# Kernel tuning notes

Hardware: AMD Instinct MI355X
Metric: run time of the kernel (lower is better)

Reference implementation:

```python
import jax, jax.numpy as jnp
import numpy as np

D_MODEL = 2048
N_HEADS = 16
D_HEAD = D_MODEL // N_HEADS
BASE = 10000.0


def _rope_cos_sin(T, d_head, base, dtype=jnp.float32):
    half = d_head // 2
    inv_freq = 1.0 / (base ** (jnp.arange(half, dtype=jnp.float32) * 2.0 / d_head))
    angles = jnp.arange(T, dtype=jnp.float32)[:, None] * inv_freq[None, :]  # [T, half]
    return jnp.cos(angles).astype(dtype), jnp.sin(angles).astype(dtype)


def _apply_rope(x, cos, sin):
    # x: [B, H, T, d_head]; cos/sin: [T, d_head//2]; interleaved pairs (0::2, 1::2)
    x1 = x[..., 0::2]
    x2 = x[..., 1::2]
    r1 = x1 * cos - x2 * sin
    r2 = x1 * sin + x2 * cos
    return jnp.stack([r1, r2], axis=-1).reshape(x.shape)


def setup_inputs() -> dict:
    key = jax.random.key(0)
    k1, k2, k3 = jax.random.split(key, 3)
    B, T = 2, 2048
    x = jax.random.normal(k1, (B, T, D_MODEL), dtype=jnp.float32)
    w_qkv = jax.random.normal(k2, (3 * D_MODEL, D_MODEL), dtype=jnp.float32) * 0.02
    w_out = jax.random.normal(k3, (D_MODEL, D_MODEL), dtype=jnp.float32) * 0.02
    return {"x": x, "w_qkv": w_qkv, "w_out": w_out}


def reference(x, w_qkv, w_out) -> jnp.ndarray:
    B, T, D = x.shape
    scale = D_HEAD ** -0.5
    qkv = jnp.einsum('btd,ed->bte', x, w_qkv)  # [B, T, 3D]
    q, k, v = jnp.split(qkv, 3, axis=-1)
    # [B, T, D] -> [B, H, T, d_head]
    q = q.reshape(B, T, N_HEADS, D_HEAD).transpose(0, 2, 1, 3)
    k = k.reshape(B, T, N_HEADS, D_HEAD).transpose(0, 2, 1, 3)
    v = v.reshape(B, T, N_HEADS, D_HEAD).transpose(0, 2, 1, 3)
    cos, sin = _rope_cos_sin(T, D_HEAD, BASE, dtype=x.dtype)
    q = _apply_rope(q, cos, sin)
    k = _apply_rope(k, cos, sin)
    scores = jnp.einsum('bhqd,bhkd->bhqk', q, k) * scale
    causal = jnp.tril(jnp.ones((T, T), dtype=bool))
    scores = jnp.where(causal, scores, jnp.finfo(scores.dtype).min)
    attn = jax.nn.softmax(scores, axis=-1)
    out = jnp.einsum('bhqk,bhkd->bhqd', attn, v)
    out = out.transpose(0, 2, 1, 3).reshape(B, T, D)
    return jnp.einsum('btd,ed->bte', out, w_out)
```

## Files before the change

### kernel.cpp

```cpp
#include <hip/hip_runtime.h>
#include <hip/hip_bf16.h>

typedef __attribute__((ext_vector_type(4))) float f32x4;
typedef __attribute__((ext_vector_type(8))) short short8;
typedef __attribute__((ext_vector_type(4))) unsigned short ushx4;

#define B_SZ 2
#define T_SZ 2048
#define H_SZ 16
#define DH 128
#define DM 2048
#define M_SZ 4096
#define N1 6144
#define KD 2048

static __device__ __forceinline__ unsigned short f2bf(float f) {
  union { float f; unsigned int u; } v; v.f = f;
  unsigned int r = v.u + 0x7fffu + ((v.u >> 16) & 1u);
  return (unsigned short)(r >> 16);
}
static __device__ __forceinline__ float bf2f(unsigned int u) {
  union { unsigned int u; float f; } v; v.u = u << 16; return v.f;
}

#define ASYNC_COPY16(gsrc, ldst) \
  __builtin_amdgcn_global_load_lds((const __attribute__((address_space(1))) void*)(gsrc), \
                                   (__attribute__((address_space(3))) void*)(ldst), 16, 0, 0)

__global__ __launch_bounds__(256) void cast_f32_bf16(const float* __restrict__ in,
                                                     unsigned short* __restrict__ out, int n4) {
  int i = blockIdx.x * 256 + threadIdx.x;
  if (i >= n4) return;
  float4 v = ((const float4*)in)[i];
  ushx4 o;
  o[0] = f2bf(v.x); o[1] = f2bf(v.y); o[2] = f2bf(v.z); o[3] = f2bf(v.w);
  ((ushx4*)out)[i] = o;
}

__global__ __launch_bounds__(64) void rope_table(float* __restrict__ cosb, float* __restrict__ sinb) {
  int t = blockIdx.x;
  int i = threadIdx.x;
  float inv = powf(10000.0f, -(float)i / 64.0f);
  float ang = (float)t * inv;
  cosb[t * 64 + i] = cosf(ang);
  sinb[t * 64 + i] = sinf(ang);
}

template <bool BF16OUT>
__global__ __launch_bounds__(256) void gemm_bt(const unsigned short* __restrict__ A,
                                               const unsigned short* __restrict__ Bt,
                                               void* __restrict__ Cout,
                                               int M, int N, int K) {
  __shared__ unsigned short As[128 * 32];
  __shared__ unsigned short Bs[128 * 32];
  const int tid = threadIdx.x;
  const int lane = tid & 63;
  const int wave = tid >> 6;
  const int wm = wave >> 1, wn = wave & 1;
  const int m0 = blockIdx.y * 128, n0 = blockIdx.x * 128;
  const int r = lane & 15, q = lane >> 4;

  f32x4 acc[4][4];
#pragma unroll
  for (int i = 0; i < 4; i++)
#pragma unroll
    for (int j = 0; j < 4; j++) acc[i][j] = (f32x4)0.0f;

  const int c0 = tid, c1 = tid + 256;
  const int row0 = c0 >> 2, kc0 = c0 & 3;
  const int row1 = c1 >> 2, kc1 = c1 & 3;

  for (int k0 = 0; k0 < K; k0 += 32) {
    __syncthreads();
    ASYNC_COPY16(A + (size_t)(m0 + row0) * K + k0 + kc0 * 8, &As[c0 * 8]);
    ASYNC_COPY16(A + (size_t)(m0 + row1) * K + k0 + kc1 * 8, &As[c1 * 8]);
    ASYNC_COPY16(Bt + (size_t)(n0 + row0) * K + k0 + kc0 * 8, &Bs[c0 * 8]);
    ASYNC_COPY16(Bt + (size_t)(n0 + row1) * K + k0 + kc1 * 8, &Bs[c1 * 8]);
    __syncthreads();

    short8 a[4], b[4];
#pragma unroll
    for (int mf = 0; mf < 4; mf++)
      a[mf] = *(const short8*)&As[(wm * 64 + mf * 16 + r) * 32 + q * 8];
#pragma unroll
    for (int nf = 0; nf < 4; nf++)
      b[nf] = *(const short8*)&Bs[(wn * 64 + nf * 16 + r) * 32 + q * 8];
#pragma unroll
    for (int mf = 0; mf < 4; mf++)
#pragma unroll
      for (int nf = 0; nf < 4; nf++)
        acc[mf][nf] = __builtin_amdgcn_mfma_f32_16x16x32_bf16(a[mf], b[nf], acc[mf][nf], 0, 0, 0);
  }

#pragma unroll
  for (int mf = 0; mf < 4; mf++) {
#pragma unroll
    for (int nf = 0; nf < 4; nf++) {
#pragma unroll
      for (int reg = 0; reg < 4; reg++) {
        int row = m0 + wm * 64 + mf * 16 + q * 4 + reg;
        int col = n0 + wn * 64 + nf * 16 + r;
        if (BF16OUT)
          ((unsigned short*)Cout)[(size_t)row * N + col] = f2bf(acc[mf][nf][reg]);
        else
          ((float*)Cout)[(size_t)row * N + col] = acc[mf][nf][reg];
      }
    }
  }
}

__global__ __launch_bounds__(256) void rope_scatter_qk(const unsigned short* __restrict__ qkv,
                                                       const float* __restrict__ cosb,
                                                       const float* __restrict__ sinb,
                                                       unsigned short* __restrict__ qb,
                                                       unsigned short* __restrict__ kb) {
  int idx = blockIdx.x * 256 + threadIdx.x;
  int m = idx >> 10;
  int p = idx & 1023;
  int h = p >> 6, i = p & 63;
  int t = m & (T_SZ - 1);
  int b = m >> 11;
  float c = cosb[t * 64 + i], s = sinb[t * 64 + i];
  size_t dst = (((size_t)(b * H_SZ + h) * T_SZ + t) * DH) + 2 * i;

  unsigned int v = *(const unsigned int*)&qkv[(size_t)m * N1 + h * DH + 2 * i];
  float x1 = bf2f(v & 0xffffu), x2 = bf2f(v >> 16);
  float r1 = x1 * c - x2 * s, r2 = x1 * s + x2 * c;
  *(unsigned int*)&qb[dst] = (unsigned int)f2bf(r1) | ((unsigned int)f2bf(r2) << 16);
  v = *(const unsigned int*)&qkv[(size_t)m * N1 + DM + h * DH + 2 * i];
  x1 = bf2f(v & 0xffffu); x2 = bf2f(v >> 16);
  r1 = x1 * c - x2 * s; r2 = x1 * s + x2 * c;
  *(unsigned int*)&kb[dst] = (unsigned int)f2bf(r1) | ((unsigned int)f2bf(r2) << 16);
}

__global__ __launch_bounds__(256) void v_transpose(const unsigned short* __restrict__ qkv,
                                                   unsigned short* __restrict__ vt) {
  __shared__ unsigned short tile[32][34];
  int bh = blockIdx.z, dblk = blockIdx.y, tblk = blockIdx.x;
  int b = bh >> 4, h = bh & 15;
  int tx = threadIdx.x & 31;
  int ty4 = threadIdx.x >> 5;
#pragma unroll
  for (int rr = 0; rr < 4; rr++) {
    int trow = ty4 * 4 + rr;
    int m = b * T_SZ + tblk * 32 + trow;
    tile[trow][tx] = qkv[(size_t)m * N1 + 2 * DM + h * DH + dblk * 32 + tx];
  }
  __syncthreads();
#pragma unroll
  for (int rr = 0; rr < 4; rr++) {
    int drow = ty4 * 4 + rr;
    vt[((size_t)bh * DH + dblk * 32 + drow) * T_SZ + tblk * 32 + tx] = tile[tx][drow];
  }
}

__global__ __launch_bounds__(256) void attn_fwd2(const unsigned short* __restrict__ qb,
                                                 const unsigned short* __restrict__ kb,
                                                 const unsigned short* __restrict__ vt,
                                                 unsigned short* __restrict__ of) {
  __shared__ unsigned short Ks[2][64 * 128];
  __shared__ unsigned short Vs[128 * 64];
  __shared__ unsigned short P_lds[4][16 * 72];

  const int tid = threadIdx.x;
  const int lane = tid & 63;
  const int w = tid >> 6;
  const int r = lane & 15, q = lane >> 4;
  const float scale = 0.08838834764831845f;

  int flat = blockIdx.x + 16 * blockIdx.y;
  int xcd = flat & 7;
  int j = flat >> 3;
  int bh = xcd * 4 + (j & 3);
  int qi = j >> 2;

  const int b = bh >> 4, h = bh & 15;
  const unsigned short* __restrict__ Qhead = qb + (size_t)bh * T_SZ * DH;
  const unsigned short* __restrict__ Kbase = kb + (size_t)bh * T_SZ * DH;
  const unsigned short* __restrict__ Vbase = vt + (size_t)bh * DH * T_SZ;

  auto stageK = [&](int kv0, int buf) {
#pragma unroll
    for (int p = 0; p < 4; p++) {
      int cc = p * 256 + tid;
      int row = cc >> 4, cr = cc & 15;
      ASYNC_COPY16(Kbase + (size_t)(kv0 + row) * DH + ((cr ^ (row & 7)) * 8),
                   &Ks[buf][cc * 8]);
    }
  };
  auto stageV = [&](int kv0) {
#pragma unroll
    for (int p = 0; p < 4; p++) {
      int cc = p * 256 + tid;
      int row = cc >> 3, cr = cc & 7;
      ASYNC_COPY16(Vbase + (size_t)row * T_SZ + kv0 + ((cr ^ (row & 7)) * 8),
                   &Vs[cc * 8]);
    }
  };

#pragma unroll 1
  for (int half = 0; half < 2; half++) {
    const int qtile = (half == 0) ? qi : (31 - qi);
    const int q0 = qtile * 64;
    const int qw = q0 + w * 16;
    const int nt = qtile + 1;

    int cur = 0;
    stageK(0, 0);

    short8 qf[4];
#pragma unroll
    for (int c = 0; c < 4; c++)
      qf[c] = *(const short8*)(Qhead + (size_t)(qw + r) * DH + c * 32 + q * 8);

    float m_run[4], l_run[4];
    f32x4 oacc[8];
#pragma unroll
    for (int i = 0; i < 4; i++) { m_run[i] = -1e30f; l_run[i] = 0.f; }
#pragma unroll
    for (int i = 0; i < 8; i++) oacc[i] = (f32x4)0.f;

#pragma unroll 1
    for (int t = 0; t < nt; t++) {
      const int kv0 = t * 64;
      stageV(kv0);
      if (t + 1 < nt) {
        stageK(kv0 + 64, cur ^ 1);
        asm volatile("s_waitcnt vmcnt(4)" ::: "memory");
      } else {
        asm volatile("s_waitcnt vmcnt(0)" ::: "memory");
      }
      __builtin_amdgcn_s_barrier();

      f32x4 S[4];
#pragma unroll
      for (int nf = 0; nf < 4; nf++) S[nf] = (f32x4)0.f;
#pragma unroll
      for (int nf = 0; nf < 4; nf++) {
#pragma unroll
        for (int c = 0; c < 4; c++) {
          short8 kf = *(const short8*)&Ks[cur][(nf * 16 + r) * 128 + (((c * 4 + q) ^ (r & 7)) * 8)];
          S[nf] = __builtin_amdgcn_mfma_f32_16x16x32_bf16(qf[c], kf, S[nf], 0, 0, 0);
        }
      }

      float Sv[4][4];
      const bool need_mask = (kv0 + 63 > qw);
#pragma unroll
      for (int nf = 0; nf < 4; nf++) {
#pragma unroll
        for (int reg = 0; reg < 4; reg++) {
          float v = S[nf][reg] * scale;
          if (need_mask) {
            int col = kv0 + nf * 16 + r;
            int row = qw + q * 4 + reg;
            if (col > row) v = -1e30f;
          }
          Sv[nf][reg] = v;
        }
      }

      float pmax[4], sc_old[4], rsum[4];
#pragma unroll
      for (int reg = 0; reg < 4; reg++) {
        float v = fmaxf(fmaxf(Sv[0][reg], Sv[1][reg]), fmaxf(Sv[2][reg], Sv[3][reg]));
#pragma unroll
        for (int s = 1; s < 16; s <<= 1) v = fmaxf(v, __shfl_xor(v, s));
        pmax[reg] = v;
      }
#pragma unroll
      for (int reg = 0; reg < 4; reg++) {
        float mn = fmaxf(m_run[reg], pmax[reg]);
        sc_old[reg] = __expf(m_run[reg] - mn);
        m_run[reg] = mn;
        rsum[reg] = 0.f;
      }
#pragma unroll
      for (int nf = 0; nf < 4; nf++) {
#pragma unroll
        for (int reg = 0; reg < 4; reg++) {
          float p = __expf(Sv[nf][reg] - m_run[reg]);
          rsum[reg] += p;
          P_lds[w][(q * 4 + reg) * 72 + nf * 16 + r] = f2bf(p);
        }
      }
#pragma unroll
      for (int reg = 0; reg < 4; reg++) {
        float v = rsum[reg];
#pragma unroll
        for (int s = 1; s < 16; s <<= 1) v += __shfl_xor(v, s);
        l_run[reg] = l_run[reg] * sc_old[reg] + v;
      }
#pragma unroll
      for (int df = 0; df < 8; df++)
#pragma unroll
        for (int reg = 0; reg < 4; reg++) oacc[df][reg] *= sc_old[reg];

      short8 pa[2];
#pragma unroll
      for (int kc = 0; kc < 2; kc++)
        pa[kc] = *(const short8*)&P_lds[w][r * 72 + kc * 32 + q * 8];
#pragma unroll
      for (int df = 0; df < 8; df++) {
#pragma unroll
        for (int kc = 0; kc < 2; kc++) {
          short8 vf = *(const short8*)&Vs[(df * 16 + r) * 64 + (((kc * 4 + q) ^ (r & 7)) * 8)];
          oacc[df] = __builtin_amdgcn_mfma_f32_16x16x32_bf16(pa[kc], vf, oacc[df], 0, 0, 0);
        }
      }

      __builtin_amdgcn_s_barrier();
      cur ^= 1;
    }

#pragma unroll
    for (int reg = 0; reg < 4; reg++) l_run[reg] = 1.0f / l_run[reg];
#pragma unroll
    for (int df = 0; df < 8; df++) {
#pragma unroll
      for (int reg = 0; reg < 4; reg++) {
        int row = qw + q * 4 + reg;
        int col = h * DH + df * 16 + r;
        of[((size_t)b * T_SZ + row) * DM + col] = f2bf(oacc[df][reg] * l_run[reg]);
      }
    }
  }
}

extern "C" void kernel_launch(void* const* d_in, const int* in_sizes, int n_in,
                              void* d_out, int out_size, void* d_ws, size_t ws_size,
                              hipStream_t stream) {
  (void)in_sizes; (void)n_in; (void)out_size; (void)ws_size;
  const float* x = (const float*)d_in[0];
  const float* w_qkv = (const float*)d_in[1];
  const float* w_out = (const float*)d_in[2];
  float* out = (float*)d_out;

  char* ws = (char*)d_ws;
  size_t off = 0;
  auto alloc = [&](size_t bytes) {
    char* p = ws + off;
    off += (bytes + 255) & ~(size_t)255;
    return p;
  };
  unsigned short* x_bf  = (unsigned short*)alloc((size_t)M_SZ * KD * 2);
  unsigned short* wq_bf = (unsigned short*)alloc((size_t)N1 * KD * 2);
  unsigned short* wo_bf = (unsigned short*)alloc((size_t)DM * KD * 2);
  unsigned short* qkv   = (unsigned short*)alloc((size_t)M_SZ * N1 * 2);
  unsigned short* qb    = (unsigned short*)alloc((size_t)B_SZ * H_SZ * T_SZ * DH * 2);
  unsigned short* kbuf  = (unsigned short*)alloc((size_t)B_SZ * H_SZ * T_SZ * DH * 2);
  unsigned short* vt    = (unsigned short*)alloc((size_t)B_SZ * H_SZ * DH * T_SZ * 2);
  unsigned short* oflat = (unsigned short*)alloc((size_t)M_SZ * DM * 2);
  float* cosb = (float*)alloc((size_t)T_SZ * 64 * 4);
  float* sinb = (float*)alloc((size_t)T_SZ * 64 * 4);

  cast_f32_bf16<<<8192, 256, 0, stream>>>(x, x_bf, M_SZ * KD / 4);
  cast_f32_bf16<<<12288, 256, 0, stream>>>(w_qkv, wq_bf, N1 * KD / 4);
  cast_f32_bf16<<<4096, 256, 0, stream>>>(w_out, wo_bf, DM * KD / 4);
  rope_table<<<T_SZ, 64, 0, stream>>>(cosb, sinb);

  gemm_bt<true><<<dim3(N1 / 128, M_SZ / 128), 256, 0, stream>>>(x_bf, wq_bf, qkv, M_SZ, N1, KD);

  rope_scatter_qk<<<16384, 256, 0, stream>>>(qkv, cosb, sinb, qb, kbuf);
  v_transpose<<<dim3(T_SZ / 32, 4, B_SZ * H_SZ), 256, 0, stream>>>(qkv, vt);

  attn_fwd2<<<dim3(16, 32), 256, 0, stream>>>(qb, kbuf, vt, oflat);

  gemm_bt<false><<<dim3(DM / 128, M_SZ / 128), 256, 0, stream>>>(oflat, wo_bf, out, M_SZ, DM, KD);
}
```

Measured before the change: 432.7 us.

## Replace GEMMs with 8-wave double-buffered ping-pong kernel using swizzled LDS and XCD remap

```diff
diff --git a/kernel.cpp b/kernel.cpp
--- a/kernel.cpp
+++ b/kernel.cpp
@@ -46,60 +46,162 @@
   sinb[t * 64 + i] = sinf(ang);
 }
 
-template <bool BF16OUT>
-__global__ __launch_bounds__(256) void gemm_bt(const unsigned short* __restrict__ A,
-                                               const unsigned short* __restrict__ Bt,
-                                               void* __restrict__ Cout,
-                                               int M, int N, int K) {
-  __shared__ unsigned short As[128 * 32];
-  __shared__ unsigned short Bs[128 * 32];
+template <int BN, bool BF16OUT>
+__global__ __launch_bounds__(512) void gemm8p(const unsigned short* __restrict__ A,
+                                              const unsigned short* __restrict__ Bt,
+                                              void* __restrict__ Cout,
+                                              int N, int nbx) {
+  constexpr int NF = BN / 64;
+  constexpr int LB = BN / 128;
+  constexpr int NT = KD / 64;
+  constexpr int WCOL = BN / 4;
+
+  __shared__ unsigned short As[2][2][256 * 32];
+  __shared__ unsigned short Bs[2][2][BN * 32];
+
   const int tid = threadIdx.x;
   const int lane = tid & 63;
-  const int wave = tid >> 6;
-  const int wm = wave >> 1, wn = wave & 1;
-  const int m0 = blockIdx.y * 128, n0 = blockIdx.x * 128;
+  const int w = tid >> 6;
+  const int wm = w >> 2, wn = w & 3;
   const int r = lane & 15, q = lane >> 4;
 
-  f32x4 acc[4][4];
-#pragma unroll
-  for (int i = 0; i < 4; i++)
-#pragma unroll
-    for (int j = 0; j < 4; j++) acc[i][j] = (f32x4)0.0f;
-
-  const int c0 = tid, c1 = tid + 256;
-  const int row0 = c0 >> 2, kc0 = c0 & 3;
-  const int row1 = c1 >> 2, kc1 = c1 & 3;
-
-  for (int k0 = 0; k0 < K; k0 += 32) {
-    __syncthreads();
-    ASYNC_COPY16(A + (size_t)(m0 + row0) * K + k0 + kc0 * 8, &As[c0 * 8]);
-    ASYNC_COPY16(A + (size_t)(m0 + row1) * K + k0 + kc1 * 8, &As[c1 * 8]);
-    ASYNC_COPY16(Bt + (size_t)(n0 + row0) * K + k0 + kc0 * 8, &Bs[c0 * 8]);
-    ASYNC_COPY16(Bt + (size_t)(n0 + row1) * K + k0 + kc1 * 8, &Bs[c1 * 8]);
-    __syncthreads();
-
-    short8 a[4], b[4];
+  const int cpx = gridDim.x >> 3;
+  const int f = (blockIdx.x & 7) * cpx + (blockIdx.x >> 3);
+  const int by = f / nbx, bx = f % nbx;
+  const int m0 = by * 256, n0 = bx * BN;
+
+  auto stageA = [&](int kt, int kh, int buf) {
+#pragma unroll
+    for (int l = 0; l < 2; l++) {
+      int cc = l * 512 + tid;
+      int row = cc >> 2, c = cc & 3;
+      ASYNC_COPY16(A + (size_t)(m0 + row) * KD + kt * 64 + kh * 32 + ((c ^ ((row >> 1) & 3)) * 8),
+                   &As[buf][kh][cc * 8]);
+    }
+  };
+  auto stageB = [&](int kt, int kh, int buf) {
+#pragma unroll
+    for (int l = 0; l < LB; l++) {
+      int cc = l * 512 + tid;
+      int row = cc >> 2, c = cc & 3;
+      ASYNC_COPY16(Bt + (size_t)(n0 + row) * KD + kt * 64 + kh * 32 + ((c ^ ((row >> 1) & 3)) * 8),
+                   &Bs[buf][kh][cc * 8]);
+    }
+  };
+
+  f32x4 acc[8][NF];
+#pragma unroll
+  for (int i = 0; i < 8; i++)
+#pragma unroll
+    for (int j = 0; j < NF; j++) acc[i][j] = (f32x4)0.0f;
+
+  short8 a[4], b[NF];
+
+  stageA(0, 0, 0); stageB(0, 0, 0); stageA(0, 1, 0); stageB(0, 1, 0);
+  if constexpr (BN == 256) asm volatile("s_waitcnt vmcnt(4)" ::: "memory");
+  else                     asm volatile("s_waitcnt vmcnt(3)" ::: "memory");
+  __builtin_amdgcn_s_barrier();
+
+#pragma unroll 1
+  for (int t = 0; t < NT; t++) {
+    const int buf = t & 1, nb = buf ^ 1;
+    const bool pf = (t + 1 < NT);
+
+#pragma unroll
+    for (int mf = 0; mf < 4; mf++) {
+      int row = wm * 128 + mf * 16 + r;
+      a[mf] = *(const short8*)&As[buf][0][row * 32 + ((q ^ ((row >> 1) & 3)) * 8)];
+    }
+#pragma unroll
+    for (int nf = 0; nf < NF; nf++) {
+      int row = wn * WCOL + nf * 16 + r;
+      b[nf] = *(const short8*)&Bs[buf][0][row * 32 + ((q ^ ((row >> 1) & 3)) * 8)];
+    }
+    if (pf) stageA(t + 1, 0, nb);
+    __builtin_amdgcn_s_barrier();
+    __builtin_amdgcn_s_setprio(1);
 #pragma unroll
     for (int mf = 0; mf < 4; mf++)
-      a[mf] = *(const short8*)&As[(wm * 64 + mf * 16 + r) * 32 + q * 8];
-#pragma unroll
-    for (int nf = 0; nf < 4; nf++)
-      b[nf] = *(const short8*)&Bs[(wn * 64 + nf * 16 + r) * 32 + q * 8];
+#pragma unroll
+      for (int nf = 0; nf < NF; nf++)
+        acc[mf][nf] = __builtin_amdgcn_mfma_f32_16x16x32_bf16(a[mf], b[nf], acc[mf][nf], 0, 0, 0);
+    __builtin_amdgcn_s_setprio(0);
+    __builtin_amdgcn_s_barrier();
+
+#pragma unroll
+    for (int mf = 0; mf < 4; mf++) {
+      int row = wm * 128 + 64 + mf * 16 + r;
+      a[mf] = *(const short8*)&As[buf][0][row * 32 + ((q ^ ((row >> 1) & 3)) * 8)];
+    }
+    if (pf) {
+      stageB(t + 1, 0, nb);
+      if constexpr (BN == 256) asm volatile("s_waitcnt vmcnt(4)" ::: "memory");
+      else                     asm volatile("s_waitcnt vmcnt(3)" ::: "memory");
+    } else {
+      asm volatile("s_waitcnt vmcnt(0)" ::: "memory");
+    }
+    __builtin_amdgcn_s_barrier();
+    __builtin_amdgcn_s_setprio(1);
 #pragma unroll
     for (int mf = 0; mf < 4; mf++)
 #pragma unroll
-      for (int nf = 0; nf < 4; nf++)
+      for (int nf = 0; nf < NF; nf++)
+        acc[4 + mf][nf] = __builtin_amdgcn_mfma_f32_16x16x32_bf16(a[mf], b[nf], acc[4 + mf][nf], 0, 0, 0);
+    __builtin_amdgcn_s_setprio(0);
+    __builtin_amdgcn_s_barrier();
+
+#pragma unroll
+    for (int mf = 0; mf < 4; mf++) {
+      int row = wm * 128 + mf * 16 + r;
+      a[mf] = *(const short8*)&As[buf][1][row * 32 + ((q ^ ((row >> 1) & 3)) * 8)];
+    }
+#pragma unroll
+    for (int nf = 0; nf < NF; nf++) {
+      int row = wn * WCOL + nf * 16 + r;
+      b[nf] = *(const short8*)&Bs[buf][1][row * 32 + ((q ^ ((row >> 1) & 3)) * 8)];
+    }
+    if (pf) stageA(t + 1, 1, nb);
+    __builtin_amdgcn_s_barrier();
+    __builtin_amdgcn_s_setprio(1);
+#pragma unroll
+    for (int mf = 0; mf < 4; mf++)
+#pragma unroll
+      for (int nf = 0; nf < NF; nf++)
         acc[mf][nf] = __builtin_amdgcn_mfma_f32_16x16x32_bf16(a[mf], b[nf], acc[mf][nf], 0, 0, 0);
+    __builtin_amdgcn_s_setprio(0);
+    __builtin_amdgcn_s_barrier();
+
+#pragma unroll
+    for (int mf = 0; mf < 4; mf++) {
+      int row = wm * 128 + 64 + mf * 16 + r;
+      a[mf] = *(const short8*)&As[buf][1][row * 32 + ((q ^ ((row >> 1) & 3)) * 8)];
+    }
+    if (pf) {
+      stageB(t + 1, 1, nb);
+      if constexpr (BN == 256) asm volatile("s_waitcnt vmcnt(4)" ::: "memory");
+      else                     asm volatile("s_waitcnt vmcnt(3)" ::: "memory");
+    } else {
+      asm volatile("s_waitcnt vmcnt(0)" ::: "memory");
+    }
+    __builtin_amdgcn_s_barrier();
+    __builtin_amdgcn_s_setprio(1);
+#pragma unroll
+    for (int mf = 0; mf < 4; mf++)
+#pragma unroll
+      for (int nf = 0; nf < NF; nf++)
+        acc[4 + mf][nf] = __builtin_amdgcn_mfma_f32_16x16x32_bf16(a[mf], b[nf], acc[4 + mf][nf], 0, 0, 0);
+    __builtin_amdgcn_s_setprio(0);
+    __builtin_amdgcn_s_barrier();
   }
 
 #pragma unroll
-  for (int mf = 0; mf < 4; mf++) {
-#pragma unroll
-    for (int nf = 0; nf < 4; nf++) {
+  for (int mf = 0; mf < 8; mf++) {
+#pragma unroll
+    for (int nf = 0; nf < NF; nf++) {
 #pragma unroll
       for (int reg = 0; reg < 4; reg++) {
-        int row = m0 + wm * 64 + mf * 16 + q * 4 + reg;
-        int col = n0 + wn * 64 + nf * 16 + r;
+        int row = m0 + wm * 128 + mf * 16 + q * 4 + reg;
+        int col = n0 + wn * WCOL + nf * 16 + r;
         if (BF16OUT)
           ((unsigned short*)Cout)[(size_t)row * N + col] = f2bf(acc[mf][nf][reg]);
         else
@@ -359,12 +461,12 @@
   cast_f32_bf16<<<4096, 256, 0, stream>>>(w_out, wo_bf, DM * KD / 4);
   rope_table<<<T_SZ, 64, 0, stream>>>(cosb, sinb);
 
-  gemm_bt<true><<<dim3(N1 / 128, M_SZ / 128), 256, 0, stream>>>(x_bf, wq_bf, qkv, M_SZ, N1, KD);
+  gemm8p<256, true><<<384, 512, 0, stream>>>(x_bf, wq_bf, qkv, N1, N1 / 256);
 
   rope_scatter_qk<<<16384, 256, 0, stream>>>(qkv, cosb, sinb, qb, kbuf);
   v_transpose<<<dim3(T_SZ / 32, 4, B_SZ * H_SZ), 256, 0, stream>>>(qkv, vt);
 
   attn_fwd2<<<dim3(16, 32), 256, 0, stream>>>(qb, kbuf, vt, oflat);
 
-  gemm_bt<false><<<dim3(DM / 128, M_SZ / 128), 256, 0, stream>>>(oflat, wo_bf, out, M_SZ, DM, KD);
-}
+  gemm8p<128, false><<<256, 512, 0, stream>>>(oflat, wo_bf, out, DM, DM / 128);
+}
```

New measurement: 414.0 us. 4.3% less time.

## Rewrite GEMMs with larger tiles, double-buffered LDS, swizzle and XCD-aware block mapping

Applied to the files above, without the earlier changes.

```diff
diff --git a/kernel.cpp b/kernel.cpp
--- a/kernel.cpp
+++ b/kernel.cpp
@@ -46,60 +46,91 @@
   sinb[t * 64 + i] = sinf(ang);
 }
 
-template <bool BF16OUT>
-__global__ __launch_bounds__(256) void gemm_bt(const unsigned short* __restrict__ A,
-                                               const unsigned short* __restrict__ Bt,
-                                               void* __restrict__ Cout,
-                                               int M, int N, int K) {
-  __shared__ unsigned short As[128 * 32];
-  __shared__ unsigned short Bs[128 * 32];
+template <int BM, int BN, bool BF16OUT>
+__global__ __launch_bounds__(512) void gemmv(const unsigned short* __restrict__ A,
+                                             const unsigned short* __restrict__ Bt,
+                                             void* __restrict__ Cout,
+                                             int N, int nbx) {
+  constexpr int NF = BN / 64;
+  constexpr int MF = BM / 32;
+  constexpr int LA = BM / 128;
+  constexpr int LB = BN / 128;
+  constexpr int NT = KD / 32;
+
+  __shared__ unsigned short As[2][BM * 32];
+  __shared__ unsigned short Bs[2][BN * 32];
+
   const int tid = threadIdx.x;
   const int lane = tid & 63;
-  const int wave = tid >> 6;
-  const int wm = wave >> 1, wn = wave & 1;
-  const int m0 = blockIdx.y * 128, n0 = blockIdx.x * 128;
+  const int w = tid >> 6;
+  const int wm = w >> 2, wn = w & 3;
   const int r = lane & 15, q = lane >> 4;
 
-  f32x4 acc[4][4];
-#pragma unroll
-  for (int i = 0; i < 4; i++)
-#pragma unroll
-    for (int j = 0; j < 4; j++) acc[i][j] = (f32x4)0.0f;
-
-  const int c0 = tid, c1 = tid + 256;
-  const int row0 = c0 >> 2, kc0 = c0 & 3;
-  const int row1 = c1 >> 2, kc1 = c1 & 3;
-
-  for (int k0 = 0; k0 < K; k0 += 32) {
+  const int cpx = gridDim.x >> 3;
+  const int f = (blockIdx.x & 7) * cpx + (blockIdx.x >> 3);
+  const int by = f / nbx, bx = f % nbx;
+  const int m0 = by * BM, n0 = bx * BN;
+
+  auto stage = [&](int kt, int buf) {
+#pragma unroll
+    for (int l = 0; l < LA; l++) {
+      int cc = l * 512 + tid;
+      int row = cc >> 2, c = cc & 3;
+      ASYNC_COPY16(A + (size_t)(m0 + row) * KD + kt * 32 + ((c ^ ((row >> 1) & 3)) * 8),
+                   &As[buf][cc * 8]);
+    }
+#pragma unroll
+    for (int l = 0; l < LB; l++) {
+      int cc = l * 512 + tid;
+      int row = cc >> 2, c = cc & 3;
+      ASYNC_COPY16(Bt + (size_t)(n0 + row) * KD + kt * 32 + ((c ^ ((row >> 1) & 3)) * 8),
+                   &Bs[buf][cc * 8]);
+    }
+  };
+
+  f32x4 acc[MF][NF];
+#pragma unroll
+  for (int i = 0; i < MF; i++)
+#pragma unroll
+    for (int j = 0; j < NF; j++) acc[i][j] = (f32x4)0.0f;
+
+  stage(0, 0);
+
+#pragma unroll 1
+  for (int t = 0; t < NT; t++) {
+    const int buf = t & 1;
     __syncthreads();
-    ASYNC_COPY16(A + (size_t)(m0 + row0) * K + k0 + kc0 * 8, &As[c0 * 8]);
-    ASYNC_COPY16(A + (size_t)(m0 + row1) * K + k0 + kc1 * 8, &As[c1 * 8]);
-    ASYNC_COPY16(Bt + (size_t)(n0 + row0) * K + k0 + kc0 * 8, &Bs[c0 * 8]);
-    ASYNC_COPY16(Bt + (size_t)(n0 + row1) * K + k0 + kc1 * 8, &Bs[c1 * 8]);
-    __syncthreads();
-
-    short8 a[4], b[4];
-#pragma unroll
-    for (int mf = 0; mf < 4; mf++)
-      a[mf] = *(const short8*)&As[(wm * 64 + mf * 16 + r) * 32 + q * 8];
-#pragma unroll
-    for (int nf = 0; nf < 4; nf++)
-      b[nf] = *(const short8*)&Bs[(wn * 64 + nf * 16 + r) * 32 + q * 8];
-#pragma unroll
-    for (int mf = 0; mf < 4; mf++)
-#pragma unroll
-      for (int nf = 0; nf < 4; nf++)
+
+    short8 a[MF], b[NF];
+#pragma unroll
+    for (int mf = 0; mf < MF; mf++) {
+      int row = wm * (BM / 2) + mf * 16 + r;
+      a[mf] = *(const short8*)&As[buf][row * 32 + ((q ^ ((row >> 1) & 3)) * 8)];
+    }
+#pragma unroll
+    for (int nf = 0; nf < NF; nf++) {
+      int row = wn * (BN / 4) + nf * 16 + r;
+      b[nf] = *(const short8*)&Bs[buf][row * 32 + ((q ^ ((row >> 1) & 3)) * 8)];
+    }
+    if (t + 1 < NT) stage(t + 1, buf ^ 1);
+
+    __builtin_amdgcn_s_setprio(1);
+#pragma unroll
+    for (int mf = 0; mf < MF; mf++)
+#pragma unroll
+      for (int nf = 0; nf < NF; nf++)
         acc[mf][nf] = __builtin_amdgcn_mfma_f32_16x16x32_bf16(a[mf], b[nf], acc[mf][nf], 0, 0, 0);
+    __builtin_amdgcn_s_setprio(0);
   }
 
 #pragma unroll
-  for (int mf = 0; mf < 4; mf++) {
-#pragma unroll
-    for (int nf = 0; nf < 4; nf++) {
+  for (int mf = 0; mf < MF; mf++) {
+#pragma unroll
+    for (int nf = 0; nf < NF; nf++) {
 #pragma unroll
       for (int reg = 0; reg < 4; reg++) {
-        int row = m0 + wm * 64 + mf * 16 + q * 4 + reg;
-        int col = n0 + wn * 64 + nf * 16 + r;
+        int row = m0 + wm * (BM / 2) + mf * 16 + q * 4 + reg;
+        int col = n0 + wn * (BN / 4) + nf * 16 + r;
         if (BF16OUT)
           ((unsigned short*)Cout)[(size_t)row * N + col] = f2bf(acc[mf][nf][reg]);
         else
@@ -359,12 +390,12 @@
   cast_f32_bf16<<<4096, 256, 0, stream>>>(w_out, wo_bf, DM * KD / 4);
   rope_table<<<T_SZ, 64, 0, stream>>>(cosb, sinb);
 
-  gemm_bt<true><<<dim3(N1 / 128, M_SZ / 128), 256, 0, stream>>>(x_bf, wq_bf, qkv, M_SZ, N1, KD);
+  gemmv<256, 256, true><<<384, 512, 0, stream>>>(x_bf, wq_bf, qkv, N1, N1 / 256);
 
   rope_scatter_qk<<<16384, 256, 0, stream>>>(qkv, cosb, sinb, qb, kbuf);
   v_transpose<<<dim3(T_SZ / 32, 4, B_SZ * H_SZ), 256, 0, stream>>>(qkv, vt);
 
   attn_fwd2<<<dim3(16, 32), 256, 0, stream>>>(qb, kbuf, vt, oflat);
 
-  gemm_bt<false><<<dim3(DM / 128, M_SZ / 128), 256, 0, stream>>>(oflat, wo_bf, out, M_SZ, DM, KD);
-}
+  gemmv<128, 256, false><<<256, 512, 0, stream>>>(oflat, wo_bf, out, DM, DM / 256);
+}
```

After: 402.8 us. 1.07x faster.
